# Optimization experiments

Measured on AMD Instinct MI355X. Metric: run time of the kernel, lower is better.

## Reference

```python
import jax, jax.numpy as jnp
import numpy as np

TEMPERATURE = 0.07
EPS = 1e-12


def setup_inputs() -> dict:
    key = jax.random.key(0)
    k1, k2 = jax.random.split(key)
    features = jax.random.normal(k1, (8192, 512), dtype=jnp.float32)
    labels = jax.random.randint(k2, (8192,), 0, 100, dtype=jnp.int64)
    return {"features": features, "labels": labels}


def reference(features, labels):
    n = features.shape[0]
    # L2 normalize along feature dim
    feats = features / jnp.linalg.norm(features, axis=1, keepdims=True)
    # positive-pair mask from labels
    mask = (labels[:, None] == labels[None, :]).astype(feats.dtype)  # [N,N]
    # scaled pairwise similarities
    logits = jnp.matmul(feats, feats.T) / TEMPERATURE  # [N,N]
    logits_max = jax.lax.stop_gradient(jnp.max(logits, axis=1, keepdims=True))
    logits = logits - logits_max
    # exclude self-similarity from denominator
    not_self = 1.0 - jnp.eye(n, dtype=feats.dtype)
    exp_logits = jnp.exp(logits) * not_self
    log_prob = logits - jnp.log(jnp.sum(exp_logits, axis=1, keepdims=True) + EPS)
    mean_log_prob_pos = jnp.sum(mask * log_prob, axis=1) / jnp.sum(mask, axis=1)
    return -jnp.mean(mean_log_prob_pos)
```

## Files before the change

### kernel.cpp

```cpp
#include <hip/hip_runtime.h>
#include <hip/hip_bf16.h>

#define NROWS 8192
#define DIM 512
#define ROWB 256
#define NCLASS 100
#define NSLICE 16
#define NT 4
#define INV_TEMP 14.285714285714286f
#define M0 14.285714285714286f
#define K2C  20.609929155556663f
#define K2CS 0.08050753576389321f
#define PSCL 0.05580357142857143f

typedef float f32x4 __attribute__((ext_vector_type(4)));
typedef int   i32x8 __attribute__((ext_vector_type(8)));

#define OFF_FB   0u
#define OFF_SP   2097152u
#define OFF_PP   2621440u
#define OFF_CNT  3145728u
#define OFF_RV   3146240u

#define AS1(p) ((const __attribute__((address_space(1))) void*)(p))
#define AS3(p) ((__attribute__((address_space(3))) void*)(p))


__global__ void norm_kernel(const float* __restrict__ F, const int* __restrict__ labels,
                            unsigned char* __restrict__ Fb, int* __restrict__ cnt) {
    __shared__ int h[NCLASS];
    if (blockIdx.x == NROWS / 4) {
        if (threadIdx.x < NCLASS) h[threadIdx.x] = 0;
        __syncthreads();
        for (int i = threadIdx.x; i < NROWS; i += 256)
            atomicAdd(&h[labels[i]], 1);
        __syncthreads();
        if (threadIdx.x < NCLASS) cnt[threadIdx.x] = h[threadIdx.x];
        return;
    }
    int row  = blockIdx.x * 4 + (threadIdx.x >> 6);
    int lane = threadIdx.x & 63;
    const float4* src = (const float4*)(F + (size_t)row * DIM);
    float4 a = src[lane * 2];
    float4 b = src[lane * 2 + 1];
    float ss = a.x*a.x + a.y*a.y + a.z*a.z + a.w*a.w
             + b.x*b.x + b.y*b.y + b.z*b.z + b.w*b.w;
    #pragma unroll
    for (int off = 32; off; off >>= 1) ss += __shfl_xor(ss, off);
    float inv = 16.0f / sqrtf(ss);
    float x[8] = {a.x*inv, a.y*inv, a.z*inv, a.w*inv,
                  b.x*inv, b.y*inv, b.z*inv, b.w*inv};
    unsigned int pk = 0;
    #pragma unroll
    for (int k = 0; k < 8; ++k) {
        float ax = fabsf(x[k]);
        unsigned c = (unsigned)(ax >= 0.25f) + (unsigned)(ax >= 0.75f)
                   + (unsigned)(ax >= 1.25f) + (unsigned)(ax >= 1.75f)
                   + (unsigned)(ax >= 2.5f)  + (unsigned)(ax >= 3.5f)
                   + (unsigned)(ax >= 5.0f);
        c |= (x[k] < 0.f) ? 8u : 0u;
        pk |= c << (k * 4);
    }
    *(unsigned int*)(Fb + (size_t)row * ROWB + lane * 4) = pk;
}

__global__ __launch_bounds__(256, 1)
void simstats_kernel(const unsigned char* __restrict__ Fb, const int* __restrict__ labels,
                     float* __restrict__ Sp, float* __restrict__ Pp) {
    __shared__ unsigned char lds[2][128][ROWB];
    __shared__ int slab[512];
    int orig  = blockIdx.x;
    int bid   = (orig & 7) * 64 + (orig >> 3);
    int strip = bid >> 4;
    int slice = bid & 15;
    int w     = threadIdx.x >> 6;
    int lane  = threadIdx.x & 63;
    int col   = lane & 15;
    int kg    = lane >> 4;
    int c7    = col & 7;
    int r0    = strip * 256 + w * 64;
    int jb0   = slice * 512;

    slab[threadIdx.x]       = labels[jb0 + threadIdx.x];
    slab[threadIdx.x + 256] = labels[jb0 + 256 + threadIdx.x];

    i32x8 afr[4][4];
    #pragma unroll
    for (int m = 0; m < 4; ++m) {
        const unsigned char* arow = Fb + (size_t)(r0 + m * 16 + col) * ROWB;
        #pragma unroll
        for (int kb = 0; kb < 4; ++kb) {
            uint4 q = *(const uint4*)(arow + kb * 64 + kg * 16);
            i32x8 v = {0, 0, 0, 0, 0, 0, 0, 0};
            v[0] = (int)q.x; v[1] = (int)q.y; v[2] = (int)q.z; v[3] = (int)q.w;
            afr[m][kb] = v;
        }
    }

    int labrow[4][4];
    #pragma unroll
    for (int m = 0; m < 4; ++m)
        #pragma unroll
        for (int r = 0; r < 4; ++r)
            labrow[m][r] = labels[r0 + m * 16 + kg * 4 + r];

    auto stage = [&](int b, int t) {
        #pragma unroll
        for (int i = 0; i < 8; ++i) {
            int nb = w * 32 + i * 4;
            int n  = nb + (lane >> 4);
            int c  = lane & 15;
            const unsigned char* src =
                Fb + (size_t)(jb0 + t * 128 + n) * ROWB + ((c ^ (n & 7)) << 4);
            __builtin_amdgcn_global_load_lds(AS1(src), AS3(&lds[b][nb][0]), 16, 0, 0);
        }
    };

    float S[4][4] = {{0.f,0.f,0.f,0.f},{0.f,0.f,0.f,0.f},
                     {0.f,0.f,0.f,0.f},{0.f,0.f,0.f,0.f}};
    float P[4][4] = {{0.f,0.f,0.f,0.f},{0.f,0.f,0.f,0.f},
                     {0.f,0.f,0.f,0.f},{0.f,0.f,0.f,0.f}};

    auto compute = [&](int b, int t) {
        #pragma unroll
        for (int ct = 0; ct < 8; ++ct) {
            const unsigned char* rowbase = &lds[b][ct * 16 + col][0];
            int lcc = slab[t * 128 + ct * 16 + col];
            f32x4 acc[4] = {{0.f,0.f,0.f,0.f},{0.f,0.f,0.f,0.f},
                            {0.f,0.f,0.f,0.f},{0.f,0.f,0.f,0.f}};
            #pragma unroll
            for (int kb = 0; kb < 4; ++kb) {
                uint4 q = *(const uint4*)(rowbase + (((kb * 4 + kg) ^ c7) << 4));
                i32x8 bop = {0, 0, 0, 0, 0, 0, 0, 0};
                bop[0] = (int)q.x; bop[1] = (int)q.y; bop[2] = (int)q.z; bop[3] = (int)q.w;
                #pragma unroll
                for (int m = 0; m < 4; ++m)
                    acc[m] = __builtin_amdgcn_mfma_scale_f32_16x16x128_f8f6f4(
                        afr[m][kb], bop, acc[m],
                        4, 4,
                        0, 0x7F7F7F7F,
                        0, 0x7F7F7F7F);
            }
            #pragma unroll
            for (int m = 0; m < 4; ++m)
                #pragma unroll
                for (int r = 0; r < 4; ++r) {
                    S[m][r] += __builtin_amdgcn_exp2f(fmaf(acc[m][r], K2CS, -K2C));
                    P[m][r] += (labrow[m][r] == lcc) ? acc[m][r] : 0.f;
                }
        }
    };

    stage(0, 0);
    for (int t = 0; t < NT; ++t) {
        __syncthreads();
        if (t + 1 < NT) stage((t + 1) & 1, t + 1);
        compute(t & 1, t);
    }

    #pragma unroll
    for (int off = 1; off < 16; off <<= 1) {
        #pragma unroll
        for (int m = 0; m < 4; ++m)
            #pragma unroll
            for (int r = 0; r < 4; ++r) {
                S[m][r] += __shfl_xor(S[m][r], off);
                P[m][r] += __shfl_xor(P[m][r], off);
            }
    }
    if (col == 0) {
        #pragma unroll
        for (int m = 0; m < 4; ++m)
            #pragma unroll
            for (int r = 0; r < 4; ++r) {
                size_t idx = (size_t)slice * NROWS + r0 + m * 16 + kg * 4 + r;
                Sp[idx] = S[m][r];
                Pp[idx] = P[m][r];
            }
    }
}

__global__ void finalize_kernel(const unsigned char* __restrict__ Fb,
                                const int* __restrict__ labels,
                                const float* __restrict__ Sp,
                                const float* __restrict__ Pp,
                                const int* __restrict__ cnt,
                                float* __restrict__ rv) {
    int i    = blockIdx.x * 4 + (threadIdx.x >> 6);
    int lane = threadIdx.x & 63;
    int lab  = labels[i];
    unsigned int pk = *(const unsigned int*)(Fb + (size_t)i * ROWB + lane * 4);
    float ssr = 0.f;
    #pragma unroll
    for (int k = 0; k < 8; ++k) {
        unsigned mth = (pk >> (k * 4)) & 7u;
        int   e    = (int)(mth >> 1);
        float half = 0.5f * (float)(mth & 1u);
        float base = e ? (1.0f + half) : half;
        float g    = base * __builtin_amdgcn_exp2f((float)(e ? e - 1 : 0));
        ssr = fmaf(g, g, ssr);
    }
    float sadd = (lane < NSLICE) ? Sp[(size_t)lane * NROWS + i] : 0.f;
    float padd = (lane < NSLICE) ? Pp[(size_t)lane * NROWS + i] : 0.f;
    #pragma unroll
    for (int off = 32; off; off >>= 1) {
        ssr  += __shfl_xor(ssr, off);
        sadd += __shfl_xor(sadd, off);
        padd += __shfl_xor(padd, off);
    }
    __shared__ float pbuf[4];
    if (lane == 0) {
        float cntf  = (float)cnt[lab];
        float eself = __builtin_amdgcn_exp2f(fmaf(ssr, K2CS, -K2C));
        float S     = sadd - eself + 1e-12f;
        pbuf[threadIdx.x >> 6] = M0 + logf(S) - (padd * PSCL) / cntf;
    }
    __syncthreads();
    if (threadIdx.x == 0) rv[blockIdx.x] = pbuf[0] + pbuf[1] + pbuf[2] + pbuf[3];
}

__global__ void reduce_kernel(const float* __restrict__ rv, float* __restrict__ out) {
    float s = 0.f;
    #pragma unroll
    for (int i = threadIdx.x; i < NROWS / 4; i += 256) s += rv[i];
    #pragma unroll
    for (int off = 32; off; off >>= 1) s += __shfl_xor(s, off);
    __shared__ float buf[4];
    int w = threadIdx.x >> 6;
    if ((threadIdx.x & 63) == 0) buf[w] = s;
    __syncthreads();
    if (threadIdx.x == 0) out[0] = (buf[0] + buf[1] + buf[2] + buf[3]) * (1.0f / (float)NROWS);
}

extern "C" void kernel_launch(void* const* d_in, const int* in_sizes, int n_in,
                              void* d_out, int out_size, void* d_ws, size_t ws_size,
                              hipStream_t stream) {
    const float* F      = (const float*)d_in[0];
    const int*   labels = (const int*)d_in[1];
    float*       out    = (float*)d_out;
    char*        ws     = (char*)d_ws;

    unsigned char* Fb   = (unsigned char*)(ws + OFF_FB);
    float*         Sp   = (float*)(ws + OFF_SP);
    float*         Pp   = (float*)(ws + OFF_PP);
    int*           cnt  = (int*)(ws + OFF_CNT);
    float*         rv   = (float*)(ws + OFF_RV);

    norm_kernel<<<NROWS / 4 + 1, 256, 0, stream>>>(F, labels, Fb, cnt);
    simstats_kernel<<<512, 256, 0, stream>>>(Fb, labels, Sp, Pp);
    finalize_kernel<<<NROWS / 4, 256, 0, stream>>>(Fb, labels, Sp, Pp, cnt, rv);
    reduce_kernel<<<1, 256, 0, stream>>>(rv, out);
}
```

Before: 54.38 us.

## Switch similarity GEMM to 32x32x64 scaled FP8/FP4 MFMA tiles

Replaces the 16x16x128 scaled MFMA with the 32x32x64 variant in the similarity-statistics kernel. Each wave now keeps two 32-row A fragments over eight k-blocks and computes four 32-column tiles per stage. The LDS swizzle widens from 8 to 16 chunks, and the label/output row mappings follow the 32x32 accumulator layout. The aim is fewer MFMA issues and fewer B-operand LDS reads per tile. The cost is a wider shuffle reduction over 32 lanes and 16-element accumulators that may raise register pressure.

```diff
diff --git a/kernel.cpp b/kernel.cpp
--- a/kernel.cpp
+++ b/kernel.cpp
@@ -13,8 +13,8 @@
 #define K2CS 0.08050753576389321f
 #define PSCL 0.05580357142857143f
 
-typedef float f32x4 __attribute__((ext_vector_type(4)));
-typedef int   i32x8 __attribute__((ext_vector_type(8)));
+typedef float f32x16 __attribute__((ext_vector_type(16)));
+typedef int   i32x8  __attribute__((ext_vector_type(8)));
 
 #define OFF_FB   0u
 #define OFF_SP   2097152u
@@ -75,34 +75,33 @@
     int slice = bid & 15;
     int w     = threadIdx.x >> 6;
     int lane  = threadIdx.x & 63;
-    int col   = lane & 15;
-    int kg    = lane >> 4;
-    int c7    = col & 7;
+    int c31   = lane & 31;
+    int hh    = lane >> 5;
     int r0    = strip * 256 + w * 64;
     int jb0   = slice * 512;
 
     slab[threadIdx.x]       = labels[jb0 + threadIdx.x];
     slab[threadIdx.x + 256] = labels[jb0 + 256 + threadIdx.x];
 
-    i32x8 afr[4][4];
-    #pragma unroll
-    for (int m = 0; m < 4; ++m) {
-        const unsigned char* arow = Fb + (size_t)(r0 + m * 16 + col) * ROWB;
-        #pragma unroll
-        for (int kb = 0; kb < 4; ++kb) {
-            uint4 q = *(const uint4*)(arow + kb * 64 + kg * 16);
+    i32x8 afr[2][8];
+    #pragma unroll
+    for (int m = 0; m < 2; ++m) {
+        const unsigned char* arow = Fb + (size_t)(r0 + m * 32 + c31) * ROWB + hh * 16;
+        #pragma unroll
+        for (int kb = 0; kb < 8; ++kb) {
+            uint4 q = *(const uint4*)(arow + kb * 32);
             i32x8 v = {0, 0, 0, 0, 0, 0, 0, 0};
             v[0] = (int)q.x; v[1] = (int)q.y; v[2] = (int)q.z; v[3] = (int)q.w;
             afr[m][kb] = v;
         }
     }
 
-    int labrow[4][4];
-    #pragma unroll
-    for (int m = 0; m < 4; ++m)
-        #pragma unroll
-        for (int r = 0; r < 4; ++r)
-            labrow[m][r] = labels[r0 + m * 16 + kg * 4 + r];
+    int labrow[2][16];
+    #pragma unroll
+    for (int m = 0; m < 2; ++m)
+        #pragma unroll
+        for (int r = 0; r < 16; ++r)
+            labrow[m][r] = labels[r0 + m * 32 + (r & 3) + 8 * (r >> 2) + 4 * hh];
 
     auto stage = [&](int b, int t) {
         #pragma unroll
@@ -111,43 +110,41 @@
             int n  = nb + (lane >> 4);
             int c  = lane & 15;
             const unsigned char* src =
-                Fb + (size_t)(jb0 + t * 128 + n) * ROWB + ((c ^ (n & 7)) << 4);
+                Fb + (size_t)(jb0 + t * 128 + n) * ROWB + ((c ^ (n & 15)) << 4);
             __builtin_amdgcn_global_load_lds(AS1(src), AS3(&lds[b][nb][0]), 16, 0, 0);
         }
     };
 
-    float S[4][4] = {{0.f,0.f,0.f,0.f},{0.f,0.f,0.f,0.f},
-                     {0.f,0.f,0.f,0.f},{0.f,0.f,0.f,0.f}};
-    float P[4][4] = {{0.f,0.f,0.f,0.f},{0.f,0.f,0.f,0.f},
-                     {0.f,0.f,0.f,0.f},{0.f,0.f,0.f,0.f}};
+    float S[2][16], P[2][16];
+    #pragma unroll
+    for (int m = 0; m < 2; ++m)
+        #pragma unroll
+        for (int r = 0; r < 16; ++r) { S[m][r] = 0.f; P[m][r] = 0.f; }
 
     auto compute = [&](int b, int t) {
         #pragma unroll
-        for (int ct = 0; ct < 8; ++ct) {
-            const unsigned char* rowbase = &lds[b][ct * 16 + col][0];
-            int lcc = slab[t * 128 + ct * 16 + col];
-            f32x4 acc[4] = {{0.f,0.f,0.f,0.f},{0.f,0.f,0.f,0.f},
-                            {0.f,0.f,0.f,0.f},{0.f,0.f,0.f,0.f}};
-            #pragma unroll
-            for (int kb = 0; kb < 4; ++kb) {
-                uint4 q = *(const uint4*)(rowbase + (((kb * 4 + kg) ^ c7) << 4));
+        for (int ct = 0; ct < 4; ++ct) {
+            const unsigned char* rowbase = &lds[b][ct * 32 + c31][0];
+            int swz = (ct * 32 + c31) & 15;
+            int lcc = slab[t * 128 + ct * 32 + c31];
+            f32x16 acc0 = {0.f}, acc1 = {0.f};
+            #pragma unroll
+            for (int kb = 0; kb < 8; ++kb) {
+                uint4 q = *(const uint4*)(rowbase + (((kb * 2 + hh) ^ swz) << 4));
                 i32x8 bop = {0, 0, 0, 0, 0, 0, 0, 0};
                 bop[0] = (int)q.x; bop[1] = (int)q.y; bop[2] = (int)q.z; bop[3] = (int)q.w;
-                #pragma unroll
-                for (int m = 0; m < 4; ++m)
-                    acc[m] = __builtin_amdgcn_mfma_scale_f32_16x16x128_f8f6f4(
-                        afr[m][kb], bop, acc[m],
-                        4, 4,
-                        0, 0x7F7F7F7F,
-                        0, 0x7F7F7F7F);
-            }
-            #pragma unroll
-            for (int m = 0; m < 4; ++m)
-                #pragma unroll
-                for (int r = 0; r < 4; ++r) {
-                    S[m][r] += __builtin_amdgcn_exp2f(fmaf(acc[m][r], K2CS, -K2C));
-                    P[m][r] += (labrow[m][r] == lcc) ? acc[m][r] : 0.f;
-                }
+                acc0 = __builtin_amdgcn_mfma_scale_f32_32x32x64_f8f6f4(
+                    afr[0][kb], bop, acc0, 4, 4, 0, 0x7F7F7F7F, 0, 0x7F7F7F7F);
+                acc1 = __builtin_amdgcn_mfma_scale_f32_32x32x64_f8f6f4(
+                    afr[1][kb], bop, acc1, 4, 4, 0, 0x7F7F7F7F, 0, 0x7F7F7F7F);
+            }
+            #pragma unroll
+            for (int r = 0; r < 16; ++r) {
+                S[0][r] += __builtin_amdgcn_exp2f(fmaf(acc0[r], K2CS, -K2C));
+                S[1][r] += __builtin_amdgcn_exp2f(fmaf(acc1[r], K2CS, -K2C));
+                P[0][r] += (labrow[0][r] == lcc) ? acc0[r] : 0.f;
+                P[1][r] += (labrow[1][r] == lcc) ? acc1[r] : 0.f;
+            }
         }
     };
 
@@ -159,21 +156,22 @@
     }
 
     #pragma unroll
-    for (int off = 1; off < 16; off <<= 1) {
-        #pragma unroll
-        for (int m = 0; m < 4; ++m)
-            #pragma unroll
-            for (int r = 0; r < 4; ++r) {
+    for (int off = 1; off < 32; off <<= 1) {
+        #pragma unroll
+        for (int m = 0; m < 2; ++m)
+            #pragma unroll
+            for (int r = 0; r < 16; ++r) {
                 S[m][r] += __shfl_xor(S[m][r], off);
                 P[m][r] += __shfl_xor(P[m][r], off);
             }
     }
-    if (col == 0) {
-        #pragma unroll
-        for (int m = 0; m < 4; ++m)
-            #pragma unroll
-            for (int r = 0; r < 4; ++r) {
-                size_t idx = (size_t)slice * NROWS + r0 + m * 16 + kg * 4 + r;
+    if (c31 == 0) {
+        #pragma unroll
+        for (int m = 0; m < 2; ++m)
+            #pragma unroll
+            for (int r = 0; r < 16; ++r) {
+                int row = r0 + m * 32 + (r & 3) + 8 * (r >> 2) + 4 * hh;
+                size_t idx = (size_t)slice * NROWS + row;
                 Sp[idx] = S[m][r];
                 Pp[idx] = P[m][r];
             }
```

Result: slower. 59.98 us (+10.3%).
